# Kernel tuning notes

Hardware: AMD Instinct MI355X
Metric: run time of the kernel (lower is better)

Reference implementation:

```python
import jax, jax.numpy as jnp
import numpy as np

NEG_SLOPE = 0.2  # PyG GATConv default leaky_relu slope


def gat_layer(x, src, dst, W, a_src, a_dst, bias, heads, out_ch, concat):
    """One GATConv layer (PyG semantics, shared lin for src/dst).
    x: [N, F_in]; src/dst: [E] int; W: [F_in, heads*out_ch];
    a_src/a_dst: [heads, out_ch]; bias: [heads*out_ch] or [out_ch]."""
    N = x.shape[0]
    h = (x @ W).reshape(N, heads, out_ch)              # [N, H, C]
    al_s = jnp.sum(h * a_src, axis=-1)                 # [N, H]
    al_d = jnp.sum(h * a_dst, axis=-1)                 # [N, H]
    e = jax.nn.leaky_relu(al_s[src] + al_d[dst], NEG_SLOPE)  # [E, H]
    # segment softmax over incoming edges of each destination node
    m = jax.ops.segment_max(e, dst, num_segments=N)
    m = jnp.where(jnp.isfinite(m), m, 0.0)             # nodes w/o edges
    ex = jnp.exp(e - m[dst])
    denom = jax.ops.segment_sum(ex, dst, num_segments=N)
    alpha = ex / denom[dst]                            # [E, H]; denom>0 via self-loops
    out = jax.ops.segment_sum(alpha[:, :, None] * h[src], dst, num_segments=N)  # [N,H,C]
    out = out.reshape(N, heads * out_ch) if concat else out.mean(axis=1)
    return out + bias


def setup_inputs() -> dict:
    key = jax.random.key(0)
    ks = jax.random.split(key, 10)
    N, E, F_in, Ch = 50000, 800000, 5, 64
    glorot = lambda k, shp: jax.random.uniform(
        k, shp, jnp.float32, -1.0, 1.0) * np.sqrt(6.0 / (shp[0] + shp[-1]))
    return {
        "x": jax.random.normal(ks[0], (N, F_in), jnp.float32),
        "edge_index": jax.random.randint(ks[1], (2, E), 0, N, jnp.int32),
        "W1": glorot(ks[2], (F_in, 4 * Ch)),
        "a_src1": glorot(ks[3], (4, Ch)),
        "a_dst1": glorot(ks[4], (4, Ch)),
        "b1": jnp.zeros((4 * Ch,), jnp.float32),
        "W2": glorot(ks[5], (4 * Ch, Ch)),
        "a_src2": glorot(ks[6], (1, Ch)),
        "a_dst2": glorot(ks[7], (1, Ch)),
        "b2": jnp.zeros((Ch,), jnp.float32),
    }


def reference(x, edge_index, W1, a_src1, a_dst1, b1, W2, a_src2, a_dst2, b2):
    N = x.shape[0]
    loops = jnp.arange(N, dtype=edge_index.dtype)      # PyG adds self-loops by default
    src = jnp.concatenate([edge_index[0], loops])
    dst = jnp.concatenate([edge_index[1], loops])
    h = gat_layer(x, src, dst, W1, a_src1, a_dst1, b1, heads=4, out_ch=64, concat=True)
    h = jax.nn.relu(h)
    h = gat_layer(h, src, dst, W2, a_src2, a_dst2, b2, heads=1, out_ch=64, concat=False)
    return h.mean(axis=0)                              # [64]
```

## Files before the change

kernel.cpp:

```cpp
#include <hip/hip_runtime.h>
#include <hip/hip_bf16.h>

#define NEG_SLOPE 0.2f

typedef __attribute__((ext_vector_type(8))) short short8;
typedef __attribute__((ext_vector_type(4))) float f32x4;

__device__ __forceinline__ float wave_sum64(float v) {
#pragma unroll
    for (int off = 32; off >= 1; off >>= 1) v += __shfl_xor(v, off, 64);
    return v;
}

__device__ __forceinline__ float bf2f(unsigned short u) {
    return __uint_as_float((unsigned int)u << 16);
}

__device__ __forceinline__ unsigned short f2bf(float f) {
    __hip_bfloat16 hb = __float2bfloat16(f);
    return *reinterpret_cast<unsigned short*>(&hb);
}

__global__ __launch_bounds__(256) void kb1_deg(
    const int* __restrict__ ei, int E, int Etot, int* __restrict__ deg) {
    int e = blockIdx.x * 256 + threadIdx.x;
    if (e >= Etot) return;
    int dst = (e < E) ? ei[E + e] : e - E;
    atomicAdd(&deg[dst], 1);
}

__global__ __launch_bounds__(256) void kb2_alloc(
    const int* __restrict__ deg, int N, int* __restrict__ counter,
    int* __restrict__ row_ptr, int* __restrict__ row_end,
    int* __restrict__ row_cur) {
    int n = blockIdx.x * 256 + threadIdx.x;
    int lane = threadIdx.x & 63;
    int d = (n < N) ? deg[n] : 0;
    int x = d;
#pragma unroll
    for (int off = 1; off < 64; off <<= 1) {
        int y = __shfl_up(x, off, 64);
        if (lane >= off) x += y;
    }
    int total = __shfl(x, 63, 64);
    int base = 0;
    if (lane == 63) base = atomicAdd(counter, total);
    base = __shfl(base, 63, 64);
    if (n < N) {
        int beg = base + x - d;
        row_ptr[n] = beg; row_cur[n] = beg; row_end[n] = beg + d;
    }
}

__global__ __launch_bounds__(256) void kb3_scatter(
    const int* __restrict__ ei, int E, int Etot,
    int* __restrict__ row_cur, int* __restrict__ csr_src) {
    int e = blockIdx.x * 256 + threadIdx.x;
    if (e >= Etot) return;
    int src, dst;
    if (e < E) { src = ei[e]; dst = ei[E + e]; }
    else       { src = dst = e - E; }
    int pos = atomicAdd(&row_cur[dst], 1);
    csr_src[pos] = src;
}

__global__ __launch_bounds__(256) void kw_pack(
    const float* __restrict__ W2, unsigned short* __restrict__ W2t) {
    int i = blockIdx.x * 256 + threadIdx.x;
    if (i >= 64 * 256) return;
    int c = i >> 8, k = i & 255;
    W2t[c * 256 + k] = f2bf(W2[k * 64 + c]);
}

__global__ __launch_bounds__(256) void kpre(
    const float* __restrict__ W1, const float* __restrict__ a_src1,
    const float* __restrict__ a_dst1, float* __restrict__ Wa_s,
    float* __restrict__ Wa_d) {
    int t = threadIdx.x;
    int h = t >> 6;
    float a_s = a_src1[t], a_d = a_dst1[t];
#pragma unroll
    for (int f = 0; f < 5; ++f) {
        float w = W1[f * 256 + t];
        float ps = wave_sum64(w * a_s);
        float pd = wave_sum64(w * a_d);
        if ((t & 63) == 0) { Wa_s[f * 4 + h] = ps; Wa_d[f * 4 + h] = pd; }
    }
}

__global__ __launch_bounds__(256) void k1p(
    const float* __restrict__ x, const float* __restrict__ Wa_s,
    const float* __restrict__ Wa_d, float* __restrict__ al_s1,
    float* __restrict__ al_d1, int N) {
    int n = blockIdx.x * 256 + threadIdx.x;
    if (n >= N) return;
    float xv[5];
#pragma unroll
    for (int f = 0; f < 5; ++f) xv[f] = x[n * 5 + f];
    float4 s = {0.f, 0.f, 0.f, 0.f}, d = {0.f, 0.f, 0.f, 0.f};
#pragma unroll
    for (int f = 0; f < 5; ++f) {
        s.x = fmaf(xv[f], Wa_s[f * 4 + 0], s.x);
        s.y = fmaf(xv[f], Wa_s[f * 4 + 1], s.y);
        s.z = fmaf(xv[f], Wa_s[f * 4 + 2], s.z);
        s.w = fmaf(xv[f], Wa_s[f * 4 + 3], s.w);
        d.x = fmaf(xv[f], Wa_d[f * 4 + 0], d.x);
        d.y = fmaf(xv[f], Wa_d[f * 4 + 1], d.y);
        d.z = fmaf(xv[f], Wa_d[f * 4 + 2], d.z);
        d.w = fmaf(xv[f], Wa_d[f * 4 + 3], d.w);
    }
    *reinterpret_cast<float4*>(&al_s1[n * 4]) = s;
    *reinterpret_cast<float4*>(&al_d1[n * 4]) = d;
}

__global__ __launch_bounds__(256) void k2_fused(
    const int* __restrict__ csr_src, const int* __restrict__ row_ptr,
    const int* __restrict__ row_end, const float* __restrict__ x,
    const float* __restrict__ al_s1, const float* __restrict__ al_d1,
    const float* __restrict__ W1, const float* __restrict__ b1,
    unsigned short* __restrict__ x2b, int N) {
    int wave = threadIdx.x >> 6, lane = threadIdx.x & 63;
    int g = lane >> 4, gl = lane & 15;
    int n = blockIdx.x * 16 + wave * 4 + g;
    bool valid = (n < N);
    int beg = valid ? row_ptr[n] : 0;
    int end = valid ? row_end[n] : 0;
    float4 ad = {0.f, 0.f, 0.f, 0.f};
    if (valid) ad = *reinterpret_cast<const float4*>(&al_d1[n * 4]);
    float agg[4][5];
#pragma unroll
    for (int h = 0; h < 4; ++h)
#pragma unroll
        for (int f = 0; f < 5; ++f) agg[h][f] = 0.f;
    float dn[4] = {0.f, 0.f, 0.f, 0.f};
    for (int base = beg; base < end; base += 16) {
        int e = base + gl;
        if (e < end) {
            int src = csr_src[e];
            const float4 as = *reinterpret_cast<const float4*>(&al_s1[src * 4]);
            float v0 = as.x + ad.x, v1 = as.y + ad.y, v2 = as.z + ad.z, v3 = as.w + ad.w;
            v0 = v0 > 0.f ? v0 : NEG_SLOPE * v0;
            v1 = v1 > 0.f ? v1 : NEG_SLOPE * v1;
            v2 = v2 > 0.f ? v2 : NEG_SLOPE * v2;
            v3 = v3 > 0.f ? v3 : NEG_SLOPE * v3;
            float ex[4];
            ex[0] = __expf(v0); ex[1] = __expf(v1); ex[2] = __expf(v2); ex[3] = __expf(v3);
            const float* xs = &x[(size_t)src * 5];
            float xv[5];
#pragma unroll
            for (int f = 0; f < 5; ++f) xv[f] = xs[f];
#pragma unroll
            for (int h = 0; h < 4; ++h) {
                dn[h] += ex[h];
#pragma unroll
                for (int f = 0; f < 5; ++f) agg[h][f] = fmaf(ex[h], xv[f], agg[h][f]);
            }
        }
    }
#pragma unroll
    for (int off = 1; off <= 8; off <<= 1) {
#pragma unroll
        for (int h = 0; h < 4; ++h) {
            dn[h] += __shfl_xor(dn[h], off, 64);
#pragma unroll
            for (int f = 0; f < 5; ++f) agg[h][f] += __shfl_xor(agg[h][f], off, 64);
        }
    }
    if (!valid) return;
    unsigned short* xo = &x2b[(size_t)n * 256];
    float rdn[4] = {1.f / dn[0], 1.f / dn[1], 1.f / dn[2], 1.f / dn[3]};
#pragma unroll
    for (int h = 0; h < 4; ++h) {
#pragma unroll
        for (int cj = 0; cj < 4; ++cj) {
            int c = cj * 16 + gl;
            float val = 0.f;
#pragma unroll
            for (int f = 0; f < 5; ++f)
                val = fmaf(agg[h][f], W1[f * 256 + h * 64 + c], val);
            float r = fmaf(val, rdn[h], b1[h * 64 + c]);
            xo[h * 64 + c] = f2bf(r > 0.f ? r : 0.f);
        }
    }
}

__global__ __launch_bounds__(256) void k3_mfma(
    const unsigned short* __restrict__ x2b, const unsigned short* __restrict__ W2t,
    const float* __restrict__ a_src2, const float* __restrict__ a_dst2,
    unsigned short* __restrict__ h2b, float* __restrict__ al_s2,
    float* __restrict__ al_d2, int N) {
    int w = threadIdx.x >> 6, l = threadIdx.x & 63;
    int m0 = blockIdx.x * 64 + w * 16;
    if (m0 >= N) return;
    int lr = l & 15, lg = l >> 4;

    short8 b0[8], b1f[8], b2f[8], b3f[8];
#pragma unroll
    for (int kk = 0; kk < 8; ++kk) {
        b0[kk]  = *reinterpret_cast<const short8*>(&W2t[(0 * 16 + lr) * 256 + kk * 32 + lg * 8]);
        b1f[kk] = *reinterpret_cast<const short8*>(&W2t[(1 * 16 + lr) * 256 + kk * 32 + lg * 8]);
        b2f[kk] = *reinterpret_cast<const short8*>(&W2t[(2 * 16 + lr) * 256 + kk * 32 + lg * 8]);
        b3f[kk] = *reinterpret_cast<const short8*>(&W2t[(3 * 16 + lr) * 256 + kk * 32 + lg * 8]);
    }
    short8 a[8];
#pragma unroll
    for (int kk = 0; kk < 8; ++kk)
        a[kk] = *reinterpret_cast<const short8*>(&x2b[(size_t)(m0 + lr) * 256 + kk * 32 + lg * 8]);

    f32x4 acc0 = {0.f, 0.f, 0.f, 0.f}, acc1 = acc0, acc2 = acc0, acc3 = acc0;
#pragma unroll
    for (int kk = 0; kk < 8; ++kk) {
        acc0 = __builtin_amdgcn_mfma_f32_16x16x32_bf16(a[kk], b0[kk],  acc0, 0, 0, 0);
        acc1 = __builtin_amdgcn_mfma_f32_16x16x32_bf16(a[kk], b1f[kk], acc1, 0, 0, 0);
        acc2 = __builtin_amdgcn_mfma_f32_16x16x32_bf16(a[kk], b2f[kk], acc2, 0, 0, 0);
        acc3 = __builtin_amdgcn_mfma_f32_16x16x32_bf16(a[kk], b3f[kk], acc3, 0, 0, 0);
    }

#pragma unroll
    for (int j = 0; j < 4; ++j) {
        unsigned short* hr = &h2b[(size_t)(m0 + lg * 4 + j) * 64];
        hr[0 * 16 + lr] = f2bf(acc0[j]);
        hr[1 * 16 + lr] = f2bf(acc1[j]);
        hr[2 * 16 + lr] = f2bf(acc2[j]);
        hr[3 * 16 + lr] = f2bf(acc3[j]);
    }

    float sA0 = a_src2[0 * 16 + lr], sA1 = a_src2[1 * 16 + lr];
    float sA2 = a_src2[2 * 16 + lr], sA3 = a_src2[3 * 16 + lr];
    float sD0 = a_dst2[0 * 16 + lr], sD1 = a_dst2[1 * 16 + lr];
    float sD2 = a_dst2[2 * 16 + lr], sD3 = a_dst2[3 * 16 + lr];
    float p0 = acc0[0] * sA0 + acc1[0] * sA1 + acc2[0] * sA2 + acc3[0] * sA3;
    float p1 = acc0[1] * sA0 + acc1[1] * sA1 + acc2[1] * sA2 + acc3[1] * sA3;
    float p2 = acc0[2] * sA0 + acc1[2] * sA1 + acc2[2] * sA2 + acc3[2] * sA3;
    float p3 = acc0[3] * sA0 + acc1[3] * sA1 + acc2[3] * sA2 + acc3[3] * sA3;
    float q0 = acc0[0] * sD0 + acc1[0] * sD1 + acc2[0] * sD2 + acc3[0] * sD3;
    float q1 = acc0[1] * sD0 + acc1[1] * sD1 + acc2[1] * sD2 + acc3[1] * sD3;
    float q2 = acc0[2] * sD0 + acc1[2] * sD1 + acc2[2] * sD2 + acc3[2] * sD3;
    float q3 = acc0[3] * sD0 + acc1[3] * sD1 + acc2[3] * sD2 + acc3[3] * sD3;
#pragma unroll
    for (int off = 1; off <= 8; off <<= 1) {
        p0 += __shfl_xor(p0, off, 64); p1 += __shfl_xor(p1, off, 64);
        p2 += __shfl_xor(p2, off, 64); p3 += __shfl_xor(p3, off, 64);
        q0 += __shfl_xor(q0, off, 64); q1 += __shfl_xor(q1, off, 64);
        q2 += __shfl_xor(q2, off, 64); q3 += __shfl_xor(q3, off, 64);
    }
    if (lr == 0) {
        int r0 = m0 + lg * 4;
        al_s2[r0 + 0] = p0; al_s2[r0 + 1] = p1; al_s2[r0 + 2] = p2; al_s2[r0 + 3] = p3;
        al_d2[r0 + 0] = q0; al_d2[r0 + 1] = q1; al_d2[r0 + 2] = q2; al_d2[r0 + 3] = q3;
    }
}

__global__ __launch_bounds__(256) void k4a_wts(
    const int* __restrict__ csr_src, const int* __restrict__ row_ptr,
    const int* __restrict__ row_end, const float* __restrict__ al_s2,
    const float* __restrict__ al_d2, float* __restrict__ ew2,
    float* __restrict__ denom2, int N) {
    int wave = threadIdx.x >> 6, lane = threadIdx.x & 63;
    int n = blockIdx.x * 4 + wave;
    if (n >= N) return;
    int beg = row_ptr[n], end = row_end[n];
    float ad = al_d2[n];
    float dsum = 0.f;
    for (int base = beg; base < end; base += 64) {
        int e = base + lane;
        if (e < end) {
            int src = csr_src[e];
            float v = al_s2[src] + ad;
            v = v > 0.f ? v : NEG_SLOPE * v;
            float ex = __expf(v);
            ew2[e] = ex;
            dsum += ex;
        }
    }
    dsum = wave_sum64(dsum);
    if (lane == 0) denom2[n] = dsum;
}

__global__ __launch_bounds__(256) void k4b_gather2(
    const int* __restrict__ csr_src, const int* __restrict__ row_ptr,
    const int* __restrict__ row_end, const unsigned short* __restrict__ h2b,
    const float* __restrict__ ew2, const float* __restrict__ denom2,
    float* __restrict__ o2, int N) {
    int wave = threadIdx.x >> 6, lane = threadIdx.x & 63;
    int n = blockIdx.x * 4 + wave;
    if (n >= N) return;
    int beg = row_ptr[n], end = row_end[n];
    float a = 0.f;
    for (int base = beg; base < end; base += 64) {
        int nn = min(64, end - base);
        int srcv = (base + lane < end) ? csr_src[base + lane] : 0;
        for (int i = 0; i < nn; ++i) {
            int src = __shfl(srcv, i, 64);
            float w = ew2[base + i];
            a = fmaf(w, bf2f(h2b[(size_t)src * 64 + lane]), a);
        }
    }
    o2[(size_t)n * 64 + lane] = a / denom2[n];
}

__global__ __launch_bounds__(64) void k5_final(
    const float* __restrict__ o2, const float* __restrict__ b2,
    float* __restrict__ out, int N) {
    int lane = threadIdx.x;
    float acc = 0.f;
    for (int n = blockIdx.x; n < N; n += gridDim.x)
        acc += o2[(size_t)n * 64 + lane];
    float v = acc * (1.f / (float)N);
    if (blockIdx.x == 0) v += b2[lane];
    atomicAdd(&out[lane], v);
}

extern "C" void kernel_launch(void* const* d_in, const int* in_sizes, int n_in,
                              void* d_out, int out_size, void* d_ws, size_t ws_size,
                              hipStream_t stream) {
    const float* x   = (const float*)d_in[0];
    const int*   ei  = (const int*)d_in[1];
    const float* W1  = (const float*)d_in[2];
    const float* as1 = (const float*)d_in[3];
    const float* ad1 = (const float*)d_in[4];
    const float* b1  = (const float*)d_in[5];
    const float* W2  = (const float*)d_in[6];
    const float* as2 = (const float*)d_in[7];
    const float* ad2 = (const float*)d_in[8];
    const float* b2  = (const float*)d_in[9];
    float* out = (float*)d_out;

    const int F_in = in_sizes[2] / 256;
    const int N = in_sizes[0] / F_in;
    const int E = in_sizes[1] / 2;
    const int Etot = E + N;

    unsigned short* x2b = (unsigned short*)d_ws;
    unsigned short* h2b = x2b + (size_t)N * 256;
    float* al_s1 = (float*)(h2b + (size_t)N * 64);
    float* al_d1 = al_s1 + (size_t)N * 4;
    float* Wa_s  = al_d1 + (size_t)N * 4;
    float* Wa_d  = Wa_s + 20;
    float* ew2   = Wa_d + 20;
    float* denom2= ew2 + (size_t)Etot;
    unsigned short* W2t = (unsigned short*)(denom2 + N);
    int* deg     = (int*)(W2t + 64 * 256);
    int* row_cur = deg + N;
    int* row_ptr = row_cur + N;
    int* row_end = row_ptr + N;
    int* counter = row_end + N;
    int* csr_src = counter + 1;
    float* o2    = (float*)x2b;
    float* al_s2 = al_s1;
    float* al_d2 = al_d1;

    hipMemsetAsync(deg, 0, (size_t)N * sizeof(int), stream);
    hipMemsetAsync(counter, 0, sizeof(int), stream);
    hipMemsetAsync(out, 0, 64 * sizeof(float), stream);

    kb1_deg    <<<(Etot + 255) / 256, 256, 0, stream>>>(ei, E, Etot, deg);
    kb2_alloc  <<<(N + 255) / 256, 256, 0, stream>>>(deg, N, counter, row_ptr, row_end, row_cur);
    kb3_scatter<<<(Etot + 255) / 256, 256, 0, stream>>>(ei, E, Etot, row_cur, csr_src);
    kw_pack    <<<64, 256, 0, stream>>>(W2, W2t);
    kpre       <<<1, 256, 0, stream>>>(W1, as1, ad1, Wa_s, Wa_d);

    k1p        <<<(N + 255) / 256, 256, 0, stream>>>(x, Wa_s, Wa_d, al_s1, al_d1, N);
    k2_fused   <<<(N + 15) / 16, 256, 0, stream>>>(csr_src, row_ptr, row_end, x, al_s1, al_d1, W1, b1, x2b, N);
    k3_mfma    <<<(N + 63) / 64, 256, 0, stream>>>(x2b, W2t, as2, ad2, h2b, al_s2, al_d2, N);
    k4a_wts    <<<(N + 3) / 4, 256, 0, stream>>>(csr_src, row_ptr, row_end, al_s2, al_d2, ew2, denom2, N);
    k4b_gather2<<<(N + 3) / 4, 256, 0, stream>>>(csr_src, row_ptr, row_end, h2b, ew2, denom2, o2, N);
    k5_final   <<<256, 64, 0, stream>>>(o2, b2, out, N);
}
```

Measured before the change: 357.6 us.

## Collapse layer-2 aggregation and node mean into per-source coefficient column sum

```diff
diff --git a/kernel.cpp b/kernel.cpp
--- a/kernel.cpp
+++ b/kernel.cpp
@@ -251,64 +251,56 @@
     }
 }
 
-__global__ __launch_bounds__(256) void k4a_wts(
-    const int* __restrict__ csr_src, const int* __restrict__ row_ptr,
-    const int* __restrict__ row_end, const float* __restrict__ al_s2,
-    const float* __restrict__ al_d2, float* __restrict__ ew2,
-    float* __restrict__ denom2, int N) {
+__global__ __launch_bounds__(256) void k4a_ew(
+    const int* __restrict__ ei, int E, int Etot,
+    const float* __restrict__ al_s2, const float* __restrict__ al_d2,
+    float* __restrict__ ew2, float* __restrict__ denom2) {
+    int e = blockIdx.x * 256 + threadIdx.x;
+    if (e >= Etot) return;
+    int src, dst;
+    if (e < E) { src = ei[e]; dst = ei[E + e]; }
+    else       { src = dst = e - E; }
+    float v = al_s2[src] + al_d2[dst];
+    v = v > 0.f ? v : NEG_SLOPE * v;
+    float ex = __expf(v);
+    ew2[e] = ex;
+    atomicAdd(&denom2[dst], ex);
+}
+
+__global__ __launch_bounds__(256) void k4b_coef(
+    const int* __restrict__ ei, int E, int Etot,
+    const float* __restrict__ ew2, const float* __restrict__ denom2,
+    float* __restrict__ C) {
+    int e = blockIdx.x * 256 + threadIdx.x;
+    if (e >= Etot) return;
+    int src, dst;
+    if (e < E) { src = ei[e]; dst = ei[E + e]; }
+    else       { src = dst = e - E; }
+    atomicAdd(&C[src], ew2[e] / denom2[dst]);
+}
+
+__global__ __launch_bounds__(256) void k4c_colsum(
+    const unsigned short* __restrict__ h2b, const float* __restrict__ C,
+    const float* __restrict__ b2, float* __restrict__ out, int N, int nblocks) {
+    __shared__ float red[4][64];
     int wave = threadIdx.x >> 6, lane = threadIdx.x & 63;
-    int n = blockIdx.x * 4 + wave;
-    if (n >= N) return;
-    int beg = row_ptr[n], end = row_end[n];
-    float ad = al_d2[n];
-    float dsum = 0.f;
-    for (int base = beg; base < end; base += 64) {
-        int e = base + lane;
-        if (e < end) {
-            int src = csr_src[e];
-            float v = al_s2[src] + ad;
-            v = v > 0.f ? v : NEG_SLOPE * v;
-            float ex = __expf(v);
-            ew2[e] = ex;
-            dsum += ex;
-        }
-    }
-    dsum = wave_sum64(dsum);
-    if (lane == 0) denom2[n] = dsum;
-}
-
-__global__ __launch_bounds__(256) void k4b_gather2(
-    const int* __restrict__ csr_src, const int* __restrict__ row_ptr,
-    const int* __restrict__ row_end, const unsigned short* __restrict__ h2b,
-    const float* __restrict__ ew2, const float* __restrict__ denom2,
-    float* __restrict__ o2, int N) {
-    int wave = threadIdx.x >> 6, lane = threadIdx.x & 63;
-    int n = blockIdx.x * 4 + wave;
-    if (n >= N) return;
-    int beg = row_ptr[n], end = row_end[n];
-    float a = 0.f;
-    for (int base = beg; base < end; base += 64) {
-        int nn = min(64, end - base);
-        int srcv = (base + lane < end) ? csr_src[base + lane] : 0;
-        for (int i = 0; i < nn; ++i) {
-            int src = __shfl(srcv, i, 64);
-            float w = ew2[base + i];
-            a = fmaf(w, bf2f(h2b[(size_t)src * 64 + lane]), a);
-        }
-    }
-    o2[(size_t)n * 64 + lane] = a / denom2[n];
-}
-
-__global__ __launch_bounds__(64) void k5_final(
-    const float* __restrict__ o2, const float* __restrict__ b2,
-    float* __restrict__ out, int N) {
-    int lane = threadIdx.x;
-    float acc = 0.f;
-    for (int n = blockIdx.x; n < N; n += gridDim.x)
-        acc += o2[(size_t)n * 64 + lane];
-    float v = acc * (1.f / (float)N);
-    if (blockIdx.x == 0) v += b2[lane];
-    atomicAdd(&out[lane], v);
+    int nw = nblocks * 4;
+    int wid = blockIdx.x * 4 + wave;
+    float a0 = 0.f, a1 = 0.f, a2 = 0.f, a3 = 0.f;
+    for (int s = wid * 4; s < N; s += nw * 4) {
+        if (s + 0 < N) a0 = fmaf(C[s + 0], bf2f(h2b[(size_t)(s + 0) * 64 + lane]), a0);
+        if (s + 1 < N) a1 = fmaf(C[s + 1], bf2f(h2b[(size_t)(s + 1) * 64 + lane]), a1);
+        if (s + 2 < N) a2 = fmaf(C[s + 2], bf2f(h2b[(size_t)(s + 2) * 64 + lane]), a2);
+        if (s + 3 < N) a3 = fmaf(C[s + 3], bf2f(h2b[(size_t)(s + 3) * 64 + lane]), a3);
+    }
+    red[wave][lane] = (a0 + a1) + (a2 + a3);
+    __syncthreads();
+    if (wave == 0) {
+        float v = red[0][lane] + red[1][lane] + red[2][lane] + red[3][lane];
+        v *= (1.f / (float)N);
+        if (blockIdx.x == 0) v += b2[lane];
+        atomicAdd(&out[lane], v);
+    }
 }
 
 extern "C" void kernel_launch(void* const* d_in, const int* in_sizes, int n_in,
@@ -339,19 +331,21 @@
     float* Wa_d  = Wa_s + 20;
     float* ew2   = Wa_d + 20;
     float* denom2= ew2 + (size_t)Etot;
-    unsigned short* W2t = (unsigned short*)(denom2 + N);
+    float* Cbuf  = denom2 + N;
+    unsigned short* W2t = (unsigned short*)(Cbuf + N);
     int* deg     = (int*)(W2t + 64 * 256);
     int* row_cur = deg + N;
     int* row_ptr = row_cur + N;
     int* row_end = row_ptr + N;
     int* counter = row_end + N;
     int* csr_src = counter + 1;
-    float* o2    = (float*)x2b;
     float* al_s2 = al_s1;
     float* al_d2 = al_d1;
 
     hipMemsetAsync(deg, 0, (size_t)N * sizeof(int), stream);
     hipMemsetAsync(counter, 0, sizeof(int), stream);
+    hipMemsetAsync(denom2, 0, (size_t)N * sizeof(float), stream);
+    hipMemsetAsync(Cbuf, 0, (size_t)N * sizeof(float), stream);
     hipMemsetAsync(out, 0, 64 * sizeof(float), stream);
 
     kb1_deg    <<<(Etot + 255) / 256, 256, 0, stream>>>(ei, E, Etot, deg);
@@ -363,7 +357,8 @@
     k1p        <<<(N + 255) / 256, 256, 0, stream>>>(x, Wa_s, Wa_d, al_s1, al_d1, N);
     k2_fused   <<<(N + 15) / 16, 256, 0, stream>>>(csr_src, row_ptr, row_end, x, al_s1, al_d1, W1, b1, x2b, N);
     k3_mfma    <<<(N + 63) / 64, 256, 0, stream>>>(x2b, W2t, as2, ad2, h2b, al_s2, al_d2, N);
-    k4a_wts    <<<(N + 3) / 4, 256, 0, stream>>>(csr_src, row_ptr, row_end, al_s2, al_d2, ew2, denom2, N);
-    k4b_gather2<<<(N + 3) / 4, 256, 0, stream>>>(csr_src, row_ptr, row_end, h2b, ew2, denom2, o2, N);
-    k5_final   <<<256, 64, 0, stream>>>(o2, b2, out, N);
-}
+    k4a_ew     <<<(Etot + 255) / 256, 256, 0, stream>>>(ei, E, Etot, al_s2, al_d2, ew2, denom2);
+    k4b_coef   <<<(Etot + 255) / 256, 256, 0, stream>>>(ei, E, Etot, ew2, denom2, Cbuf);
+    const int K4C_BLOCKS = 128;
+    k4c_colsum <<<K4C_BLOCKS, 256, 0, stream>>>(h2b, Cbuf, b2, out, N, K4C_BLOCKS);
+}
```

Result: no change. 363.5 us (+1.7%).
